# Kernel optimization log

Measured on AMD Instinct MI355X. Metric: run time of the kernel, lower is better.

Reference implementation:

```python
import jax, jax.numpy as jnp
import numpy as np

B, S, H, D = 4, 2048, 16, 128

def setup_inputs() -> dict:
    key = jax.random.key(0)
    kq, kk, kv = jax.random.split(key, 3)
    shape = (B, S, H, D)
    return {
        "q": jax.random.normal(kq, shape, dtype=jnp.float32),
        "k": jax.random.normal(kk, shape, dtype=jnp.float32),
        "v": jax.random.normal(kv, shape, dtype=jnp.float32),
    }

def reference(q, k, v):
    # Fused recurrent linear attention (causal, unnormalized):
    #   H_t = H_{t-1} + k_t v_t^T ;  o_t = (scale * q_t) @ H_t
    scale = jnp.asarray(q.shape[-1], q.dtype) ** -0.5
    # move seq axis to front for scan: [S, B, H, D]
    qs = jnp.moveaxis(q, 1, 0) * scale
    ks = jnp.moveaxis(k, 1, 0)
    vs = jnp.moveaxis(v, 1, 0)

    def step(h, qkv):
        qt, kt, vt = qkv  # each [B, H, D]
        h = h + kt[..., :, None] * vt[..., None, :]  # [B, H, Dk, Dv]
        o = jnp.einsum('bhk,bhkv->bhv', qt, h)       # [B, H, Dv]
        return h, o

    h0 = jnp.zeros((q.shape[0], q.shape[2], q.shape[3], v.shape[3]), dtype=q.dtype)
    _, o = jax.lax.scan(step, h0, (qs, ks, vs))
    return jnp.moveaxis(o, 0, 1)  # [B, S, H, D]
```

## Files before the change

### kernel.cpp

```cpp
#include <hip/hip_runtime.h>


#define Bc 4
#define Sq 2048
#define Hh 16
#define Dd 128
#define RS (Hh * Dd)
#define Cc 128
#define NCH (Sq / Cc)
#define BHt (Bc * Hh)
#define NSEG 4
#define CPS (NCH / NSEG)
#define SCALE 0.08838834764831845f

using frag_ab = __attribute__((ext_vector_type(8))) short;
using frag_cd = __attribute__((ext_vector_type(4))) float;

__device__ __forceinline__ unsigned short f2bf(float f) {
  union { float f; unsigned u; } x; x.f = f;
  unsigned r = x.u + 0x7FFFu + ((x.u >> 16) & 1u);
  return (unsigned short)(r >> 16);
}
__device__ __forceinline__ float bf2f(unsigned short u) {
  union { unsigned u; float f; } x; x.u = ((unsigned)u) << 16;
  return x.f;
}
__device__ __forceinline__ int sw64(int r, int c) {
  return r * 64 + ((((c >> 3) ^ (r & 7)) << 3) | (c & 7));
}
__device__ __forceinline__ int sw128(int r, int c) {
  return r * 128 + ((((c >> 3) ^ (r & 15)) << 3) | (c & 7));
}
__device__ __forceinline__ int swKT(int dk, int t) {
  return dk * 128 + ((((t >> 3) ^ (dk ^ (dk >> 4))) & 15) << 3) + (t & 7);
}
__device__ __forceinline__ int swVT(int dv, int t) {
  return dv * 128 + ((((t >> 3) ^ dv) & 15) << 3) + (t & 7);
}

__global__ __launch_bounds__(256) void phA_state(const float* __restrict__ kg,
                                                 const float* __restrict__ vg,
                                                 unsigned short* __restrict__ st) {
  __shared__ unsigned short KT[128 * 128];
  __shared__ unsigned short VT[16 * 128];
  const int tid = threadIdx.x;
  const int bh = blockIdx.x & 63;
  const int slice = (blockIdx.x >> 6) & 7;
  const int seg = blockIdx.x >> 9;
  const int b = bh >> 4, h = bh & 15;
  const int dv0 = slice * 16;
  const size_t base = (size_t)b * Sq * RS + (size_t)h * Dd;
  const int w = tid >> 6, L = tid & 63, li = L & 15, q4 = L >> 4;
  const int kdk0 = (tid & 31) * 4;
  const int ktg4 = (tid >> 5) * 4;
  const int vdv0l = (tid & 3) * 4;
  const int vt0 = (tid >> 2) * 2;

  float4 rk[4][4];
  float4 rv[2];
  auto prefetch = [&](int n) {
    const size_t t0g = (size_t)n * Cc;
#pragma unroll
    for (int p = 0; p < 4; ++p) {
      const int t0 = p * 32 + ktg4;
#pragma unroll
      for (int i = 0; i < 4; ++i)
        rk[p][i] = *(const float4*)(kg + base + (t0g + t0 + i) * (size_t)RS + kdk0);
    }
#pragma unroll
    for (int i = 0; i < 2; ++i)
      rv[i] = *(const float4*)(vg + base + (t0g + vt0 + i) * (size_t)RS + dv0 + vdv0l);
  };

  frag_cd acc[2];
  acc[0] = (frag_cd){0.f, 0.f, 0.f, 0.f};
  acc[1] = (frag_cd){0.f, 0.f, 0.f, 0.f};
  const int n0 = seg * CPS;
  prefetch(n0);
  const size_t sbb = (size_t)bh * NCH * (128 * 128);

  auto store_acc = [&](int slot) {
    const size_t sb = sbb + (size_t)slot * (128 * 128);
#pragma unroll
    for (int nt = 0; nt < 2; ++nt)
#pragma unroll
      for (int r = 0; r < 4; ++r) {
        const int dv = dv0 + 4 * q4 + r;
        const int dk = 32 * w + 16 * nt + li;
        st[sb + (size_t)dv * 128 + dk] = f2bf(acc[nt][r]);
      }
  };

  for (int j = 0; j < CPS; ++j) {
    __syncthreads();
#pragma unroll
    for (int p = 0; p < 4; ++p) {
      const int t0 = p * 32 + ktg4;
#pragma unroll
      for (int jj = 0; jj < 4; ++jj) {
        ushort4 u;
        u.x = f2bf(((const float*)&rk[p][0])[jj]);
        u.y = f2bf(((const float*)&rk[p][1])[jj]);
        u.z = f2bf(((const float*)&rk[p][2])[jj]);
        u.w = f2bf(((const float*)&rk[p][3])[jj]);
        *(ushort4*)&KT[swKT(kdk0 + jj, t0)] = u;
      }
    }
#pragma unroll
    for (int jj = 0; jj < 4; ++jj) {
      ushort2 u;
      u.x = f2bf(((const float*)&rv[0])[jj]);
      u.y = f2bf(((const float*)&rv[1])[jj]);
      *(ushort2*)&VT[swVT(vdv0l + jj, vt0)] = u;
    }
    if (j + 1 < CPS) prefetch(n0 + j + 1);
    __syncthreads();
    if (j > 0) store_acc(n0 + j);
#pragma unroll
    for (int kt = 0; kt < 4; ++kt) {
      frag_ab af = *(const frag_ab*)&VT[swVT(li, 32 * kt + 8 * q4)];
#pragma unroll
      for (int nt = 0; nt < 2; ++nt) {
        frag_ab bf = *(const frag_ab*)&KT[swKT(32 * w + 16 * nt + li, 32 * kt + 8 * q4)];
        acc[nt] = __builtin_amdgcn_mfma_f32_16x16x32_bf16(af, bf, acc[nt], 0, 0, 0);
      }
    }
  }
  if (seg + 1 < NSEG) store_acc(n0);
}

__global__ __launch_bounds__(256, 4) void phB_out(const float* __restrict__ qg,
                                                  const float* __restrict__ kg,
                                                  const float* __restrict__ vg,
                                                  const unsigned short* __restrict__ st,
                                                  float* __restrict__ o) {
  __shared__ unsigned short QP[64 * 128];
  __shared__ unsigned short Bb[128 * 64];
  const int tid = threadIdx.x;
  const int bid = blockIdx.x;
  const int bh = bid & 63, n = (bid >> 6) & 15, tb = bid >> 10;
  const int b = bh >> 4, h = bh & 15;
  const size_t cbase = (size_t)b * Sq * RS + (size_t)n * Cc * RS + (size_t)h * Dd;
  const size_t tbase = cbase + (size_t)(64 * tb) * RS;
  const size_t sbh = (size_t)bh * NCH * (128 * 128);
  const int sseg = n >> 2, jj = n & 3;
  const int nmat = sseg + (jj ? 1 : 0);
  const int w = tid >> 6, L = tid & 63;
  const int wr = w >> 1, wc = w & 1, li = L & 15, q4 = L >> 4;

#pragma unroll
  for (int it = 0; it < 8; ++it) {
    const int f = it * 256 + tid;
    const int t = f >> 5;
    const int c0 = (f & 31) << 2;
    const float4 q4v = *(const float4*)(qg + tbase + (size_t)t * RS + c0);
    ushort4 qu;
    qu.x = f2bf(q4v.x * SCALE); qu.y = f2bf(q4v.y * SCALE);
    qu.z = f2bf(q4v.z * SCALE); qu.w = f2bf(q4v.w * SCALE);
    *(ushort4*)&QP[sw128(t, c0)] = qu;
  }
  frag_cd accO[2][4], accP[2][4];
#pragma unroll
  for (int i = 0; i < 2; ++i)
#pragma unroll
    for (int j = 0; j < 4; ++j) {
      accO[i][j] = (frag_cd){0.f, 0.f, 0.f, 0.f};
      accP[i][j] = (frag_cd){0.f, 0.f, 0.f, 0.f};
    }

  if (nmat > 0) {
    for (int half = 0; half < 2; ++half) {
      __syncthreads();
      if (nmat == 1) {
        const int slot = sseg ? 0 : n;
#pragma unroll
        for (int it = 0; it < 4; ++it) {
          const int f = it * 256 + tid;
          const int dv = f >> 3;
          const int c8 = (f & 7) << 3;
          const uint4 hv = *(const uint4*)(st + sbh + ((size_t)slot << 14) +
                                           (size_t)dv * 128 + 64 * half + c8);
          *(uint4*)&Bb[sw64(dv, c8)] = hv;
        }
      } else {
#pragma unroll
        for (int it = 0; it < 4; ++it) {
          const int f = it * 256 + tid;
          const int dv = f >> 3;
          const int c8 = (f & 7) << 3;
          float s8[8];
#pragma unroll
          for (int e = 0; e < 8; ++e) s8[e] = 0.f;
          for (int m = 0; m < nmat; ++m) {
            const int slot = (m < sseg) ? (m << 2) : n;
            const uint4 hv = *(const uint4*)(st + sbh + ((size_t)slot << 14) +
                                             (size_t)dv * 128 + 64 * half + c8);
            const unsigned hw[4] = {hv.x, hv.y, hv.z, hv.w};
#pragma unroll
            for (int e = 0; e < 4; ++e) {
              s8[2 * e + 0] += bf2f((unsigned short)(hw[e] & 0xFFFFu));
              s8[2 * e + 1] += bf2f((unsigned short)(hw[e] >> 16));
            }
          }
          unsigned pk[4];
#pragma unroll
          for (int e = 0; e < 4; ++e)
            pk[e] = (unsigned)f2bf(s8[2 * e]) | ((unsigned)f2bf(s8[2 * e + 1]) << 16);
          uint4 hv; hv.x = pk[0]; hv.y = pk[1]; hv.z = pk[2]; hv.w = pk[3];
          *(uint4*)&Bb[sw64(dv, c8)] = hv;
        }
      }
      __syncthreads();
#pragma unroll
      for (int kt = 0; kt < 2; ++kt) {
        const int ktg = 2 * half + kt;
        frag_ab af[2], bf_[4];
#pragma unroll
        for (int mt = 0; mt < 2; ++mt)
          af[mt] = *(const frag_ab*)&QP[sw128(32 * wr + 16 * mt + li, 32 * ktg + 8 * q4)];
#pragma unroll
        for (int nt = 0; nt < 4; ++nt)
          bf_[nt] = *(const frag_ab*)&Bb[sw64(64 * wc + 16 * nt + li, 32 * kt + 8 * q4)];
#pragma unroll
        for (int mt = 0; mt < 2; ++mt)
#pragma unroll
          for (int nt = 0; nt < 4; ++nt)
            accO[mt][nt] = __builtin_amdgcn_mfma_f32_16x16x32_bf16(af[mt], bf_[nt], accO[mt][nt], 0, 0, 0);
      }
    }
  }

  for (int half = 0; half < 2; ++half) {
    __syncthreads();
    if (tb) {
#pragma unroll
      for (int it = 0; it < 8; ++it) {
        const int f = it * 256 + tid;
        const int t = f >> 4;
        const int c0 = (f & 15) << 2;
        const float4 k4v = *(const float4*)(kg + cbase + (size_t)t * RS + 64 * half + c0);
        ushort4 ku;
        ku.x = f2bf(k4v.x); ku.y = f2bf(k4v.y); ku.z = f2bf(k4v.z); ku.w = f2bf(k4v.w);
        *(ushort4*)&Bb[sw64(t, c0)] = ku;
      }
    } else {
#pragma unroll
      for (int it = 0; it < 4; ++it) {
        const int f = it * 256 + tid;
        const int t = f >> 4;
        const int c0 = (f & 15) << 2;
        const float4 k4v = *(const float4*)(kg + cbase + (size_t)t * RS + 64 * half + c0);
        ushort4 ku;
        ku.x = f2bf(k4v.x); ku.y = f2bf(k4v.y); ku.z = f2bf(k4v.z); ku.w = f2bf(k4v.w);
        *(ushort4*)&Bb[sw64(t, c0)] = ku;
      }
    }
    __syncthreads();
    if (64 * wc <= 64 * tb + 32 * wr + 31) {
#pragma unroll
      for (int kt = 0; kt < 2; ++kt) {
        const int ktg = 2 * half + kt;
        frag_ab af[2], bf_[4];
#pragma unroll
        for (int mt = 0; mt < 2; ++mt)
          af[mt] = *(const frag_ab*)&QP[sw128(32 * wr + 16 * mt + li, 32 * ktg + 8 * q4)];
#pragma unroll
        for (int nt = 0; nt < 4; ++nt)
          bf_[nt] = *(const frag_ab*)&Bb[sw64(64 * wc + 16 * nt + li, 32 * kt + 8 * q4)];
#pragma unroll
        for (int mt = 0; mt < 2; ++mt)
#pragma unroll
          for (int nt = 0; nt < 4; ++nt)
            if (64 * wc + 16 * nt <= 64 * tb + 32 * wr + 16 * mt + 15)
              accP[mt][nt] = __builtin_amdgcn_mfma_f32_16x16x32_bf16(af[mt], bf_[nt], accP[mt][nt], 0, 0, 0);
      }
    }
  }
  __syncthreads();
#pragma unroll
  for (int mt = 0; mt < 2; ++mt)
#pragma unroll
    for (int nt = 0; nt < 4; ++nt) {
      const int t0 = 32 * wr + 16 * mt + 4 * q4;
      const int s = 64 * wc + 16 * nt + li;
#pragma unroll
      for (int r = 0; r < 4; ++r) {
        const int t = t0 + r;
        QP[sw128(t, s)] = (s <= t + 64 * tb) ? f2bf(accP[mt][nt][r]) : (unsigned short)0;
      }
    }

  const int nh2 = tb ? 2 : 1;
  for (int half = 0; half < nh2; ++half) {
    __syncthreads();
#pragma unroll
    for (int it = 0; it < 8; ++it) {
      const int sl = (tid & 15) | ((it & 3) << 4);
      const int c0 = ((tid >> 4) | ((it >> 2) << 4)) << 2;
      const int s = 64 * half + sl;
      const float4 v4v = *(const float4*)(vg + cbase + (size_t)s * RS + c0);
      Bb[sw64(c0 + 0, sl)] = f2bf(v4v.x);
      Bb[sw64(c0 + 1, sl)] = f2bf(v4v.y);
      Bb[sw64(c0 + 2, sl)] = f2bf(v4v.z);
      Bb[sw64(c0 + 3, sl)] = f2bf(v4v.w);
    }
    __syncthreads();
#pragma unroll
    for (int kt = 0; kt < 2; ++kt) {
      const int ktg = 2 * half + kt;
      if (32 * ktg > 64 * tb + 32 * wr + 31) continue;
      frag_ab af[2], bf_[4];
#pragma unroll
      for (int mt = 0; mt < 2; ++mt)
        af[mt] = *(const frag_ab*)&QP[sw128(32 * wr + 16 * mt + li, 32 * ktg + 8 * q4)];
#pragma unroll
      for (int nt = 0; nt < 4; ++nt)
        bf_[nt] = *(const frag_ab*)&Bb[sw64(64 * wc + 16 * nt + li, 32 * kt + 8 * q4)];
#pragma unroll
      for (int mt = 0; mt < 2; ++mt)
#pragma unroll
        for (int nt = 0; nt < 4; ++nt)
          if (32 * ktg <= 64 * tb + 32 * wr + 16 * mt + 15)
            accO[mt][nt] = __builtin_amdgcn_mfma_f32_16x16x32_bf16(af[mt], bf_[nt], accO[mt][nt], 0, 0, 0);
    }
  }
#pragma unroll
  for (int mt = 0; mt < 2; ++mt)
#pragma unroll
    for (int nt = 0; nt < 4; ++nt)
#pragma unroll
      for (int r = 0; r < 4; ++r) {
        const int t = 32 * wr + 16 * mt + 4 * q4 + r;
        const int dv = 64 * wc + 16 * nt + li;
        o[tbase + (size_t)t * RS + dv] = accO[mt][nt][r];
      }
}

extern "C" void kernel_launch(void* const* d_in, const int* in_sizes, int n_in,
                              void* d_out, int out_size, void* d_ws, size_t ws_size,
                              hipStream_t stream) {
  const float* q = (const float*)d_in[0];
  const float* k = (const float*)d_in[1];
  const float* v = (const float*)d_in[2];
  float* o = (float*)d_out;
  unsigned short* st = (unsigned short*)d_ws;
  hipLaunchKernelGGL(phA_state, dim3(BHt * 8 * NSEG), dim3(256), 0, stream, k, v, st);
  hipLaunchKernelGGL(phB_out, dim3(BHt * NCH * 2), dim3(256), 0, stream, q, k, v, st, o);
}
```

Before: 284.0 us.

## Double-buffer output-phase tiles and halve state segment count

Adds a second LDS staging buffer in the output kernel so the global loads of K, V and state tiles are issued into registers while the MFMA work on the previous tile runs, replacing the serial load-sync-compute sequence. It also cuts state segments from 4 to 2, so each chunk sums at most two prefix matrices. The segment cut lengthens the sequential state-scan phase and the extra buffer and registers lower the occupancy bound from 4 to 3 blocks.

After: 320.1 us. 12.7% more time.

```diff
diff --git a/kernel.cpp b/kernel.cpp
--- a/kernel.cpp
+++ b/kernel.cpp
@@ -9,7 +9,7 @@
 #define Cc 128
 #define NCH (Sq / Cc)
 #define BHt (Bc * Hh)
-#define NSEG 4
+#define NSEG 2
 #define CPS (NCH / NSEG)
 #define SCALE 0.08838834764831845f
 
@@ -129,13 +129,13 @@
   if (seg + 1 < NSEG) store_acc(n0);
 }
 
-__global__ __launch_bounds__(256, 4) void phB_out(const float* __restrict__ qg,
+__global__ __launch_bounds__(256, 3) void phB_out(const float* __restrict__ qg,
                                                   const float* __restrict__ kg,
                                                   const float* __restrict__ vg,
                                                   const unsigned short* __restrict__ st,
                                                   float* __restrict__ o) {
   __shared__ unsigned short QP[64 * 128];
-  __shared__ unsigned short Bb[128 * 64];
+  __shared__ unsigned short Bb[2][128 * 64];
   const int tid = threadIdx.x;
   const int bid = blockIdx.x;
   const int bh = bid & 63, n = (bid >> 6) & 15, tb = bid >> 10;
@@ -143,22 +143,11 @@
   const size_t cbase = (size_t)b * Sq * RS + (size_t)n * Cc * RS + (size_t)h * Dd;
   const size_t tbase = cbase + (size_t)(64 * tb) * RS;
   const size_t sbh = (size_t)bh * NCH * (128 * 128);
-  const int sseg = n >> 2, jj = n & 3;
+  const int sseg = n >> 3, jj = n & 7;
   const int nmat = sseg + (jj ? 1 : 0);
   const int w = tid >> 6, L = tid & 63;
   const int wr = w >> 1, wc = w & 1, li = L & 15, q4 = L >> 4;
 
-#pragma unroll
-  for (int it = 0; it < 8; ++it) {
-    const int f = it * 256 + tid;
-    const int t = f >> 5;
-    const int c0 = (f & 31) << 2;
-    const float4 q4v = *(const float4*)(qg + tbase + (size_t)t * RS + c0);
-    ushort4 qu;
-    qu.x = f2bf(q4v.x * SCALE); qu.y = f2bf(q4v.y * SCALE);
-    qu.z = f2bf(q4v.z * SCALE); qu.w = f2bf(q4v.w * SCALE);
-    *(ushort4*)&QP[sw128(t, c0)] = qu;
-  }
   frag_cd accO[2][4], accP[2][4];
 #pragma unroll
   for (int i = 0; i < 2; ++i)
@@ -168,49 +157,112 @@
       accP[i][j] = (frag_cd){0.f, 0.f, 0.f, 0.f};
     }
 
-  if (nmat > 0) {
-    for (int half = 0; half < 2; ++half) {
-      __syncthreads();
+  float4 sA[8], sB[8];
+  uint4 hA[2][4], hB[2][4];
+
+  auto loadK = [&](int half, float4 (&s)[8]) {
+#pragma unroll
+    for (int it = 0; it < 8; ++it) {
+      const int f = it * 256 + tid;
+      const int t = f >> 4;
+      const int c0 = (f & 15) << 2;
+      s[it] = *(const float4*)(kg + cbase + (size_t)t * RS + 64 * half + c0);
+    }
+  };
+  auto writeK = [&](const float4 (&s)[8], unsigned short* bb) {
+#pragma unroll
+    for (int it = 0; it < 8; ++it) {
+      const int f = it * 256 + tid;
+      const int t = f >> 4;
+      const int c0 = (f & 15) << 2;
+      ushort4 ku;
+      ku.x = f2bf(s[it].x); ku.y = f2bf(s[it].y);
+      ku.z = f2bf(s[it].z); ku.w = f2bf(s[it].w);
+      *(ushort4*)&bb[sw64(t, c0)] = ku;
+    }
+  };
+  auto loadV = [&](int half, float4 (&s)[8]) {
+#pragma unroll
+    for (int it = 0; it < 8; ++it) {
+      const int sl = (tid & 15) | ((it & 3) << 4);
+      const int c0 = ((tid >> 4) | ((it >> 2) << 4)) << 2;
+      const int sd = 64 * half + sl;
+      s[it] = *(const float4*)(vg + cbase + (size_t)sd * RS + c0);
+    }
+  };
+  auto writeV = [&](const float4 (&s)[8], unsigned short* bb) {
+#pragma unroll
+    for (int it = 0; it < 8; ++it) {
+      const int sl = (tid & 15) | ((it & 3) << 4);
+      const int c0 = ((tid >> 4) | ((it >> 2) << 4)) << 2;
+      bb[sw64(c0 + 0, sl)] = f2bf(s[it].x);
+      bb[sw64(c0 + 1, sl)] = f2bf(s[it].y);
+      bb[sw64(c0 + 2, sl)] = f2bf(s[it].z);
+      bb[sw64(c0 + 3, sl)] = f2bf(s[it].w);
+    }
+  };
+  auto loadH = [&](int half, uint4 (&hr)[2][4]) {
+#pragma unroll
+    for (int m = 0; m < 2; ++m) {
+      if (m >= nmat) break;
+      const int slot = (m < sseg) ? 0 : n;
+#pragma unroll
+      for (int it = 0; it < 4; ++it) {
+        const int f = it * 256 + tid;
+        const int dv = f >> 3;
+        const int c8 = (f & 7) << 3;
+        hr[m][it] = *(const uint4*)(st + sbh + ((size_t)slot << 14) +
+                                    (size_t)dv * 128 + 64 * half + c8);
+      }
+    }
+  };
+  auto writeH = [&](const uint4 (&hr)[2][4], unsigned short* bb) {
+#pragma unroll
+    for (int it = 0; it < 4; ++it) {
+      const int f = it * 256 + tid;
+      const int dv = f >> 3;
+      const int c8 = (f & 7) << 3;
+      uint4 out;
       if (nmat == 1) {
-        const int slot = sseg ? 0 : n;
-#pragma unroll
-        for (int it = 0; it < 4; ++it) {
-          const int f = it * 256 + tid;
-          const int dv = f >> 3;
-          const int c8 = (f & 7) << 3;
-          const uint4 hv = *(const uint4*)(st + sbh + ((size_t)slot << 14) +
-                                           (size_t)dv * 128 + 64 * half + c8);
-          *(uint4*)&Bb[sw64(dv, c8)] = hv;
+        out = hr[0][it];
+      } else {
+        const unsigned a[4] = {hr[0][it].x, hr[0][it].y, hr[0][it].z, hr[0][it].w};
+        const unsigned c[4] = {hr[1][it].x, hr[1][it].y, hr[1][it].z, hr[1][it].w};
+        unsigned pk[4];
+#pragma unroll
+        for (int e = 0; e < 4; ++e) {
+          const float lo = bf2f((unsigned short)(a[e] & 0xFFFFu)) +
+                           bf2f((unsigned short)(c[e] & 0xFFFFu));
+          const float hi = bf2f((unsigned short)(a[e] >> 16)) +
+                           bf2f((unsigned short)(c[e] >> 16));
+          pk[e] = (unsigned)f2bf(lo) | ((unsigned)f2bf(hi) << 16);
         }
-      } else {
-#pragma unroll
-        for (int it = 0; it < 4; ++it) {
-          const int f = it * 256 + tid;
-          const int dv = f >> 3;
-          const int c8 = (f & 7) << 3;
-          float s8[8];
-#pragma unroll
-          for (int e = 0; e < 8; ++e) s8[e] = 0.f;
-          for (int m = 0; m < nmat; ++m) {
-            const int slot = (m < sseg) ? (m << 2) : n;
-            const uint4 hv = *(const uint4*)(st + sbh + ((size_t)slot << 14) +
-                                             (size_t)dv * 128 + 64 * half + c8);
-            const unsigned hw[4] = {hv.x, hv.y, hv.z, hv.w};
-#pragma unroll
-            for (int e = 0; e < 4; ++e) {
-              s8[2 * e + 0] += bf2f((unsigned short)(hw[e] & 0xFFFFu));
-              s8[2 * e + 1] += bf2f((unsigned short)(hw[e] >> 16));
-            }
-          }
-          unsigned pk[4];
-#pragma unroll
-          for (int e = 0; e < 4; ++e)
-            pk[e] = (unsigned)f2bf(s8[2 * e]) | ((unsigned)f2bf(s8[2 * e + 1]) << 16);
-          uint4 hv; hv.x = pk[0]; hv.y = pk[1]; hv.z = pk[2]; hv.w = pk[3];
-          *(uint4*)&Bb[sw64(dv, c8)] = hv;
-        }
-      }
-      __syncthreads();
+        out.x = pk[0]; out.y = pk[1]; out.z = pk[2]; out.w = pk[3];
+      }
+      *(uint4*)&bb[sw64(dv, c8)] = out;
+    }
+  };
+
+  auto gemmO = [&](const unsigned short* bb, int half) {
+#pragma unroll
+    for (int kt = 0; kt < 2; ++kt) {
+      const int ktg = 2 * half + kt;
+      frag_ab af[2], bf_[4];
+#pragma unroll
+      for (int mt = 0; mt < 2; ++mt)
+        af[mt] = *(const frag_ab*)&QP[sw128(32 * wr + 16 * mt + li, 32 * ktg + 8 * q4)];
+#pragma unroll
+      for (int nt = 0; nt < 4; ++nt)
+        bf_[nt] = *(const frag_ab*)&bb[sw64(64 * wc + 16 * nt + li, 32 * kt + 8 * q4)];
+#pragma unroll
+      for (int mt = 0; mt < 2; ++mt)
+#pragma unroll
+        for (int nt = 0; nt < 4; ++nt)
+          accO[mt][nt] = __builtin_amdgcn_mfma_f32_16x16x32_bf16(af[mt], bf_[nt], accO[mt][nt], 0, 0, 0);
+    }
+  };
+  auto gemmP = [&](const unsigned short* bb, int half) {
+    if (64 * wc <= 64 * tb + 32 * wr + 31) {
 #pragma unroll
       for (int kt = 0; kt < 2; ++kt) {
         const int ktg = 2 * half + kt;
@@ -220,53 +272,7 @@
           af[mt] = *(const frag_ab*)&QP[sw128(32 * wr + 16 * mt + li, 32 * ktg + 8 * q4)];
 #pragma unroll
         for (int nt = 0; nt < 4; ++nt)
-          bf_[nt] = *(const frag_ab*)&Bb[sw64(64 * wc + 16 * nt + li, 32 * kt + 8 * q4)];
-#pragma unroll
-        for (int mt = 0; mt < 2; ++mt)
-#pragma unroll
-          for (int nt = 0; nt < 4; ++nt)
-            accO[mt][nt] = __builtin_amdgcn_mfma_f32_16x16x32_bf16(af[mt], bf_[nt], accO[mt][nt], 0, 0, 0);
-      }
-    }
-  }
-
-  for (int half = 0; half < 2; ++half) {
-    __syncthreads();
-    if (tb) {
-#pragma unroll
-      for (int it = 0; it < 8; ++it) {
-        const int f = it * 256 + tid;
-        const int t = f >> 4;
-        const int c0 = (f & 15) << 2;
-        const float4 k4v = *(const float4*)(kg + cbase + (size_t)t * RS + 64 * half + c0);
-        ushort4 ku;
-        ku.x = f2bf(k4v.x); ku.y = f2bf(k4v.y); ku.z = f2bf(k4v.z); ku.w = f2bf(k4v.w);
-        *(ushort4*)&Bb[sw64(t, c0)] = ku;
-      }
-    } else {
-#pragma unroll
-      for (int it = 0; it < 4; ++it) {
-        const int f = it * 256 + tid;
-        const int t = f >> 4;
-        const int c0 = (f & 15) << 2;
-        const float4 k4v = *(const float4*)(kg + cbase + (size_t)t * RS + 64 * half + c0);
-        ushort4 ku;
-        ku.x = f2bf(k4v.x); ku.y = f2bf(k4v.y); ku.z = f2bf(k4v.z); ku.w = f2bf(k4v.w);
-        *(ushort4*)&Bb[sw64(t, c0)] = ku;
-      }
-    }
-    __syncthreads();
-    if (64 * wc <= 64 * tb + 32 * wr + 31) {
-#pragma unroll
-      for (int kt = 0; kt < 2; ++kt) {
-        const int ktg = 2 * half + kt;
-        frag_ab af[2], bf_[4];
-#pragma unroll
-        for (int mt = 0; mt < 2; ++mt)
-          af[mt] = *(const frag_ab*)&QP[sw128(32 * wr + 16 * mt + li, 32 * ktg + 8 * q4)];
-#pragma unroll
-        for (int nt = 0; nt < 4; ++nt)
-          bf_[nt] = *(const frag_ab*)&Bb[sw64(64 * wc + 16 * nt + li, 32 * kt + 8 * q4)];
+          bf_[nt] = *(const frag_ab*)&bb[sw64(64 * wc + 16 * nt + li, 32 * kt + 8 * q4)];
 #pragma unroll
         for (int mt = 0; mt < 2; ++mt)
 #pragma unroll
@@ -275,36 +281,8 @@
               accP[mt][nt] = __builtin_amdgcn_mfma_f32_16x16x32_bf16(af[mt], bf_[nt], accP[mt][nt], 0, 0, 0);
       }
     }
-  }
-  __syncthreads();
-#pragma unroll
-  for (int mt = 0; mt < 2; ++mt)
-#pragma unroll
-    for (int nt = 0; nt < 4; ++nt) {
-      const int t0 = 32 * wr + 16 * mt + 4 * q4;
-      const int s = 64 * wc + 16 * nt + li;
-#pragma unroll
-      for (int r = 0; r < 4; ++r) {
-        const int t = t0 + r;
-        QP[sw128(t, s)] = (s <= t + 64 * tb) ? f2bf(accP[mt][nt][r]) : (unsigned short)0;
-      }
-    }
-
-  const int nh2 = tb ? 2 : 1;
-  for (int half = 0; half < nh2; ++half) {
-    __syncthreads();
-#pragma unroll
-    for (int it = 0; it < 8; ++it) {
-      const int sl = (tid & 15) | ((it & 3) << 4);
-      const int c0 = ((tid >> 4) | ((it >> 2) << 4)) << 2;
-      const int s = 64 * half + sl;
-      const float4 v4v = *(const float4*)(vg + cbase + (size_t)s * RS + c0);
-      Bb[sw64(c0 + 0, sl)] = f2bf(v4v.x);
-      Bb[sw64(c0 + 1, sl)] = f2bf(v4v.y);
-      Bb[sw64(c0 + 2, sl)] = f2bf(v4v.z);
-      Bb[sw64(c0 + 3, sl)] = f2bf(v4v.w);
-    }
-    __syncthreads();
+  };
+  auto gemmV = [&](const unsigned short* bb, int half) {
 #pragma unroll
     for (int kt = 0; kt < 2; ++kt) {
       const int ktg = 2 * half + kt;
@@ -315,7 +293,7 @@
         af[mt] = *(const frag_ab*)&QP[sw128(32 * wr + 16 * mt + li, 32 * ktg + 8 * q4)];
 #pragma unroll
       for (int nt = 0; nt < 4; ++nt)
-        bf_[nt] = *(const frag_ab*)&Bb[sw64(64 * wc + 16 * nt + li, 32 * kt + 8 * q4)];
+        bf_[nt] = *(const frag_ab*)&bb[sw64(64 * wc + 16 * nt + li, 32 * kt + 8 * q4)];
 #pragma unroll
       for (int mt = 0; mt < 2; ++mt)
 #pragma unroll
@@ -323,7 +301,91 @@
           if (32 * ktg <= 64 * tb + 32 * wr + 16 * mt + 15)
             accO[mt][nt] = __builtin_amdgcn_mfma_f32_16x16x32_bf16(af[mt], bf_[nt], accO[mt][nt], 0, 0, 0);
     }
+  };
+  auto pwrite = [&]() {
+#pragma unroll
+    for (int mt = 0; mt < 2; ++mt)
+#pragma unroll
+      for (int nt = 0; nt < 4; ++nt) {
+        const int t0 = 32 * wr + 16 * mt + 4 * q4;
+        const int s = 64 * wc + 16 * nt + li;
+#pragma unroll
+        for (int r = 0; r < 4; ++r) {
+          const int t = t0 + r;
+          QP[sw128(t, s)] = (s <= t + 64 * tb) ? f2bf(accP[mt][nt][r]) : (unsigned short)0;
+        }
+      }
+  };
+
+  {
+    float4 qr[8];
+#pragma unroll
+    for (int it = 0; it < 8; ++it) {
+      const int f = it * 256 + tid;
+      const int t = f >> 5;
+      const int c0 = (f & 31) << 2;
+      qr[it] = *(const float4*)(qg + tbase + (size_t)t * RS + c0);
+    }
+    loadK(0, sA);
+#pragma unroll
+    for (int it = 0; it < 8; ++it) {
+      const int f = it * 256 + tid;
+      const int t = f >> 5;
+      const int c0 = (f & 31) << 2;
+      ushort4 qu;
+      qu.x = f2bf(qr[it].x * SCALE); qu.y = f2bf(qr[it].y * SCALE);
+      qu.z = f2bf(qr[it].z * SCALE); qu.w = f2bf(qr[it].w * SCALE);
+      *(ushort4*)&QP[sw128(t, c0)] = qu;
+    }
+    loadK(1, sB);
+    writeK(sA, Bb[0]);
   }
+  __syncthreads();
+
+  if (nmat) {
+    loadH(0, hA);
+    writeK(sB, Bb[1]);
+    gemmP(Bb[0], 0);
+    __syncthreads();
+    loadH(1, hB);
+    writeH(hA, Bb[0]);
+    gemmP(Bb[1], 1);
+    __syncthreads();
+    loadV(0, sA);
+    writeH(hB, Bb[1]);
+    gemmO(Bb[0], 0);
+    __syncthreads();
+    if (tb) loadV(1, sB);
+    writeV(sA, Bb[0]);
+    gemmO(Bb[1], 1);
+    __syncthreads();
+    pwrite();
+    __syncthreads();
+    if (tb) writeV(sB, Bb[1]);
+    gemmV(Bb[0], 0);
+    if (tb) {
+      __syncthreads();
+      gemmV(Bb[1], 1);
+    }
+  } else {
+    loadV(0, sA);
+    writeK(sB, Bb[1]);
+    gemmP(Bb[0], 0);
+    __syncthreads();
+    if (tb) loadV(1, sB);
+    writeV(sA, Bb[0]);
+    gemmP(Bb[1], 1);
+    __syncthreads();
+    pwrite();
+    __syncthreads();
+    if (tb) writeV(sB, Bb[1]);
+    gemmV(Bb[0], 0);
+    if (tb) {
+      __syncthreads();
+      gemmV(Bb[1], 1);
+    }
+  }
+
 #pragma unroll
   for (int mt = 0; mt < 2; ++mt)
 #pragma unroll
```
